# Kernel tuning notes

Measured on AMD Instinct MI355X. Metric: run time of the kernel, lower is better.

Reference implementation:

```python
import jax, jax.numpy as jnp
import numpy as np

WINDOW = 1024
HOP = 256

def setup_inputs() -> dict:
    key = jax.random.key(0)
    X = jax.random.normal(key, (16, 2, 262144), dtype=jnp.float32)
    return {"X": X}

def reference(X):
    # X: (B, 2, T) with channel 0 = Re, channel 1 = Im.
    # Identity-weight Conv1d(1, window, kernel=window, stride=hop) is exactly
    # strided framing: frame t is X[..., t*hop : t*hop + window].
    B, _, T = X.shape
    n_frames = (T - WINDOW) // HOP + 1
    # (n_frames, WINDOW) gather index into the time axis
    idx = jnp.arange(n_frames)[:, None] * HOP + jnp.arange(WINDOW)[None, :]
    frames = X[:, :, idx]                      # (B, 2, n_frames, WINDOW)
    return jnp.transpose(frames, (0, 1, 3, 2)) # (B, 2, WINDOW, n_frames)
```

## Files before the change

### kernel.cpp

```cpp
#include <hip/hip_runtime.h>

#define WINDOW_SZ 1024
#define HOP_SZ    256
#define NFRAMES   1021
#define T_LEN     262144

#define FT 64
#define WT 64
#define LDS_STRIDE 65

__global__ __launch_bounds__(256)
void frame_transpose_kernel(const float* __restrict__ X,
                            float* __restrict__ out) {
    __shared__ float lds[WT * LDS_STRIDE];

    const int tid = threadIdx.x;
    const int f0  = blockIdx.x * FT;
    const int w0  = blockIdx.y * WT;
    const int bc  = blockIdx.z;

    const float* Xbc = X + (size_t)bc * T_LEN;

    {
        const int j = tid & 15;
        int seg     = tid >> 4;
#pragma unroll
        for (int p = 0; p < 4; ++p, seg += 16) {
            const int f = f0 + seg;
            if (f < NFRAMES) {
                const float4 v = *(const float4*)(Xbc + (size_t)f * HOP_SZ + w0 + 4 * j);
                const int wl = 4 * j;
                lds[(wl + 0) * LDS_STRIDE + seg] = v.x;
                lds[(wl + 1) * LDS_STRIDE + seg] = v.y;
                lds[(wl + 2) * LDS_STRIDE + seg] = v.z;
                lds[(wl + 3) * LDS_STRIDE + seg] = v.w;
            }
        }
    }

    __syncthreads();

    {
        const int fl = tid & 63;
        const int wg = tid >> 6;
        const int f  = f0 + fl;
        if (f < NFRAMES) {
            float* obase = out + ((size_t)bc * WINDOW_SZ + (w0 + wg * 16)) * (size_t)NFRAMES + f;
#pragma unroll
            for (int r = 0; r < 16; ++r) {
                obase[(size_t)r * NFRAMES] = lds[(wg * 16 + r) * LDS_STRIDE + fl];
            }
        }
    }
}

extern "C" void kernel_launch(void* const* d_in, const int* in_sizes, int n_in,
                              void* d_out, int out_size, void* d_ws, size_t ws_size,
                              hipStream_t stream) {
    const float* X = (const float*)d_in[0];
    float* out = (float*)d_out;

    dim3 block(256, 1, 1);
    dim3 grid((NFRAMES + FT - 1) / FT,
              WINDOW_SZ / WT,
              32);
    frame_transpose_kernel<<<grid, block, 0, stream>>>(X, out);
}
```

Measured before the change: 167.9 us.

## Vectorize LDS transpose with 4x4 register blocks and remap blocks across XCDs

Each thread now loads four consecutive frames as float4s, transposes them as a 4x4 register block, and writes float4 vectors into LDS using a padded stride of 68. The output phase issues unaligned float4 global stores, each covering four frames, in place of scalar stores. The launch becomes a flat 1D grid with a swizzle that spreads neighbouring work tiles across the 8 XCDs. Together these aim to cut LDS and global memory instruction counts and improve L2 locality. The risks are misaligned vector stores, because NFRAMES is odd, and possible LDS bank conflicts at the new stride.

```diff
diff --git a/kernel.cpp b/kernel.cpp
--- a/kernel.cpp
+++ b/kernel.cpp
@@ -7,48 +7,69 @@
 
 #define FT 64
 #define WT 64
-#define LDS_STRIDE 65
+#define S  68
+
+typedef float f4a __attribute__((ext_vector_type(4)));
+typedef float f4u __attribute__((ext_vector_type(4), aligned(4)));
 
 __global__ __launch_bounds__(256)
 void frame_transpose_kernel(const float* __restrict__ X,
                             float* __restrict__ out) {
-    __shared__ float lds[WT * LDS_STRIDE];
+    __shared__ float lds[WT * S];
+
+    const int bid  = blockIdx.x;
+    const int work = ((bid & 7) << 10) | (bid >> 3);
+    const int xt   = work & 15;
+    const int yt   = (work >> 4) & 15;
+    const int bc   = work >> 8;
 
     const int tid = threadIdx.x;
-    const int f0  = blockIdx.x * FT;
-    const int w0  = blockIdx.y * WT;
-    const int bc  = blockIdx.z;
+    const int f0  = xt * FT;
+    const int w0  = yt * WT;
 
     const float* Xbc = X + (size_t)bc * T_LEN;
 
+    const int j = tid & 15;
+    const int g = tid >> 4;
+
     {
-        const int j = tid & 15;
-        int seg     = tid >> 4;
-#pragma unroll
-        for (int p = 0; p < 4; ++p, seg += 16) {
-            const int f = f0 + seg;
-            if (f < NFRAMES) {
-                const float4 v = *(const float4*)(Xbc + (size_t)f * HOP_SZ + w0 + 4 * j);
-                const int wl = 4 * j;
-                lds[(wl + 0) * LDS_STRIDE + seg] = v.x;
-                lds[(wl + 1) * LDS_STRIDE + seg] = v.y;
-                lds[(wl + 2) * LDS_STRIDE + seg] = v.z;
-                lds[(wl + 3) * LDS_STRIDE + seg] = v.w;
-            }
+        const float* src = Xbc + (size_t)(f0 + 4 * g) * HOP_SZ + w0 + 4 * j;
+        float4 v0, v1, v2, v3;
+        if (f0 + 4 * g + 3 < NFRAMES) {
+            v0 = *(const float4*)(src);
+            v1 = *(const float4*)(src + HOP_SZ);
+            v2 = *(const float4*)(src + 2 * HOP_SZ);
+            v3 = *(const float4*)(src + 3 * HOP_SZ);
+        } else {
+            v0 = v1 = v2 = v3 = float4{0.f, 0.f, 0.f, 0.f};
+            if (f0 + 4 * g + 0 < NFRAMES) v0 = *(const float4*)(src);
+            if (f0 + 4 * g + 1 < NFRAMES) v1 = *(const float4*)(src + HOP_SZ);
+            if (f0 + 4 * g + 2 < NFRAMES) v2 = *(const float4*)(src + 2 * HOP_SZ);
         }
+        float* row = &lds[(4 * j) * S + 4 * g];
+        *(f4a*)(row        ) = f4a{v0.x, v1.x, v2.x, v3.x};
+        *(f4a*)(row + S    ) = f4a{v0.y, v1.y, v2.y, v3.y};
+        *(f4a*)(row + 2 * S) = f4a{v0.z, v1.z, v2.z, v3.z};
+        *(f4a*)(row + 3 * S) = f4a{v0.w, v1.w, v2.w, v3.w};
     }
 
     __syncthreads();
 
     {
-        const int fl = tid & 63;
-        const int wg = tid >> 6;
-        const int f  = f0 + fl;
-        if (f < NFRAMES) {
-            float* obase = out + ((size_t)bc * WINDOW_SZ + (w0 + wg * 16)) * (size_t)NFRAMES + f;
+        const int q  = tid & 15;
+        const int wl = tid >> 4;
+        const int fq = f0 + 4 * q;
+        float* obase = out + ((size_t)bc * WINDOW_SZ + (w0 + wl)) * (size_t)NFRAMES + fq;
+        if (fq + 3 < NFRAMES) {
 #pragma unroll
-            for (int r = 0; r < 16; ++r) {
-                obase[(size_t)r * NFRAMES] = lds[(wg * 16 + r) * LDS_STRIDE + fl];
+            for (int r = 0; r < 4; ++r) {
+                f4a t = *(const f4a*)&lds[(wl + 16 * r) * S + 4 * q];
+                *(f4u*)(obase + (size_t)(16 * r) * NFRAMES) = (f4u)t;
+            }
+        } else if (fq < NFRAMES) {
+#pragma unroll
+            for (int r = 0; r < 4; ++r) {
+                obase[(size_t)(16 * r) * NFRAMES] = lds[(wl + 16 * r) * S + 4 * q];
             }
         }
     }
@@ -61,8 +82,6 @@
     float* out = (float*)d_out;
 
     dim3 block(256, 1, 1);
-    dim3 grid((NFRAMES + FT - 1) / FT,
-              WINDOW_SZ / WT,
-              32);
+    dim3 grid(16 * 16 * 32, 1, 1);
     frame_transpose_kernel<<<grid, block, 0, stream>>>(X, out);
 }
```

After: 165.1 us. No clear change (-1.7%).

## Stage full 16-row output region in LDS and write contiguous vectorized nontemporal stores

Applied to the files above, without the earlier changes.

Each block now handles 16 window rows across all 1021 frames, staging a 16x1021 region (about 65 KB) in LDS. Because that region is contiguous in the output, it can be written with fully coalesced float4 nontemporal stores instead of row-strided scalar stores. Block indices are swizzled so consecutive blocks spread across batch and window offsets, and the block size rises to 512 threads. The large LDS footprint limits occupancy, the LDS writes of stride NFRAMES may cause bank conflicts, and a 16-byte output store alignment is assumed.

```diff
diff --git a/kernel.cpp b/kernel.cpp
--- a/kernel.cpp
+++ b/kernel.cpp
@@ -5,35 +5,42 @@
 #define NFRAMES   1021
 #define T_LEN     262144
 
-#define FT 64
-#define WT 64
-#define LDS_STRIDE 65
+#define WROWS 16
+#define REGION (WROWS * NFRAMES)
+#define NPASS_LD 8
+#define NVEC4 (REGION / 4)
 
-__global__ __launch_bounds__(256)
+typedef float f4 __attribute__((ext_vector_type(4)));
+
+__global__ __launch_bounds__(512)
 void frame_transpose_kernel(const float* __restrict__ X,
                             float* __restrict__ out) {
-    __shared__ float lds[WT * LDS_STRIDE];
+    __shared__ float lds[REGION];
+
+    const int bid  = blockIdx.x;
+    const int work = ((bid & 7) << 8) | (bid >> 3);
+    const int bc    = work >> 6;
+    const int wt    = work & 63;
+    const int outer = wt >> 2;
+    const int inner = wt & 3;
+    const int w0    = inner * 256 + outer * 16;
 
     const int tid = threadIdx.x;
-    const int f0  = blockIdx.x * FT;
-    const int w0  = blockIdx.y * WT;
-    const int bc  = blockIdx.z;
-
     const float* Xbc = X + (size_t)bc * T_LEN;
 
     {
-        const int j = tid & 15;
-        int seg     = tid >> 4;
+        const int q  = tid & 3;
+        const int fo = tid >> 2;
+        const int wl = 4 * q;
 #pragma unroll
-        for (int p = 0; p < 4; ++p, seg += 16) {
-            const int f = f0 + seg;
+        for (int p = 0; p < NPASS_LD; ++p) {
+            const int f = p * 128 + fo;
             if (f < NFRAMES) {
-                const float4 v = *(const float4*)(Xbc + (size_t)f * HOP_SZ + w0 + 4 * j);
-                const int wl = 4 * j;
-                lds[(wl + 0) * LDS_STRIDE + seg] = v.x;
-                lds[(wl + 1) * LDS_STRIDE + seg] = v.y;
-                lds[(wl + 2) * LDS_STRIDE + seg] = v.z;
-                lds[(wl + 3) * LDS_STRIDE + seg] = v.w;
+                const f4 v = *(const f4*)(Xbc + (size_t)f * HOP_SZ + w0 + wl);
+                lds[(wl + 0) * NFRAMES + f] = v.x;
+                lds[(wl + 1) * NFRAMES + f] = v.y;
+                lds[(wl + 2) * NFRAMES + f] = v.z;
+                lds[(wl + 3) * NFRAMES + f] = v.w;
             }
         }
     }
@@ -41,14 +48,13 @@
     __syncthreads();
 
     {
-        const int fl = tid & 63;
-        const int wg = tid >> 6;
-        const int f  = f0 + fl;
-        if (f < NFRAMES) {
-            float* obase = out + ((size_t)bc * WINDOW_SZ + (w0 + wg * 16)) * (size_t)NFRAMES + f;
+        float* obase = out + (size_t)(bc * WINDOW_SZ + w0) * NFRAMES;
 #pragma unroll
-            for (int r = 0; r < 16; ++r) {
-                obase[(size_t)r * NFRAMES] = lds[(wg * 16 + r) * LDS_STRIDE + fl];
+        for (int p = 0; p < 8; ++p) {
+            const int idx = p * 512 + tid;
+            if (idx < NVEC4) {
+                const f4 t = *(const f4*)&lds[4 * idx];
+                __builtin_nontemporal_store(t, (f4*)(obase + 4 * (size_t)idx));
             }
         }
     }
@@ -60,9 +66,7 @@
     const float* X = (const float*)d_in[0];
     float* out = (float*)d_out;
 
-    dim3 block(256, 1, 1);
-    dim3 grid((NFRAMES + FT - 1) / FT,
-              WINDOW_SZ / WT,
-              32);
+    dim3 block(512, 1, 1);
+    dim3 grid(32 * 64, 1, 1);
     frame_transpose_kernel<<<grid, block, 0, stream>>>(X, out);
 }
```

Result: slower. 176.2 us (+4.9%).
